# Kernel tuning notes

Hardware: AMD Instinct MI355X
Metric: run time of the kernel (lower is better)

Reference implementation:

```python
import jax, jax.numpy as jnp
import numpy as np

B, H, V, L = 4096, 1024, 64, 16  # batch, hidden_size, msg_vocsize, max_msg_len


def setup_inputs() -> dict:
    key = jax.random.key(0)
    ks = jax.random.split(key, 10)
    s = 1.0 / np.sqrt(H)
    return {
        "encoder_hidden": jax.random.normal(ks[0], (B, H), jnp.float32),
        "encoder_cell": jax.random.normal(ks[1], (B, H), jnp.float32),
        "W_ih": jax.random.uniform(ks[2], (4 * H, H), jnp.float32, -s, s),
        "W_hh": jax.random.uniform(ks[3], (4 * H, H), jnp.float32, -s, s),
        "b_ih": jax.random.uniform(ks[4], (4 * H,), jnp.float32, -s, s),
        "b_hh": jax.random.uniform(ks[5], (4 * H,), jnp.float32, -s, s),
        "W_out": jax.random.uniform(ks[6], (V, H), jnp.float32, -s, s),
        "b_out": jax.random.uniform(ks[7], (V,), jnp.float32, -s, s),
        "init_input": jnp.zeros((1, H), jnp.float32),  # nn.Parameter initialized to zeros
        "msg_embedding": jax.random.normal(ks[8], (V, H), jnp.float32),
    }


def reference(encoder_hidden, encoder_cell, W_ih, W_hh, b_ih, b_hh,
              W_out, b_out, init_input, msg_embedding):
    batch = encoder_hidden.shape[0]
    x0 = jnp.broadcast_to(init_input, (batch, H))

    def step(carry, _):
        h, c, x, logp = carry
        x = jax.nn.relu(x)
        gates = x @ W_ih.T + b_ih + h @ W_hh.T + b_hh  # [B, 4H]
        i, f, g, o = jnp.split(gates, 4, axis=-1)      # torch LSTMCell gate order
        i, f, o = jax.nn.sigmoid(i), jax.nn.sigmoid(f), jax.nn.sigmoid(o)
        g = jnp.tanh(g)
        c = f * c + i * g
        h = o * jnp.tanh(c)
        logits = h @ W_out.T + b_out                   # [B, V]
        probs = jax.nn.softmax(logits, axis=1)
        pred = jax.nn.one_hot(jnp.argmax(probs, axis=1), V, dtype=probs.dtype)
        logp = logp + jnp.log(jnp.sum(probs * pred, axis=1))
        x = pred @ msg_embedding                       # [B, H]
        return (h, c, x, logp), (pred, logits)

    init = (encoder_hidden, encoder_cell, x0, jnp.zeros((batch,), encoder_hidden.dtype))
    (_, _, _, log_probs), (message, digits) = jax.lax.scan(step, init, None, length=L)
    mask = jnp.ones((L, 1, batch), encoder_hidden.dtype)
    return message, mask, digits, log_probs
```

## Files before the change

### kernel.cpp

```cpp
#include <hip/hip_runtime.h>
#include <math.h>

#define HD    1024
#define BATCH 4096
#define VOC   64
#define MSGL  16
#define KH    1024
#define NG    4096

typedef _Float16 f16;
typedef _Float16 f16x8 __attribute__((ext_vector_type(8)));
typedef _Float16 f16x4 __attribute__((ext_vector_type(4)));
typedef float    f32x4 __attribute__((ext_vector_type(4)));

__device__ __forceinline__ void splt(float v, f16& hi, f16& lo) {
    f16 h = (f16)v;
    hi = h;
    lo = (f16)(v - (float)h);
}

__device__ __forceinline__ float sigm_f(float x) {
    return __builtin_amdgcn_rcpf(1.0f + __builtin_amdgcn_exp2f(-1.44269504088896f * x));
}
__device__ __forceinline__ float tanh_f(float x) {
    return 1.0f - 2.0f * __builtin_amdgcn_rcpf(1.0f + __builtin_amdgcn_exp2f(2.88539008177793f * x));
}

__device__ __forceinline__ int orig_n(int np) {
    const int bxx = np >> 8, rem = np & 255;
    const int jh = rem >> 6, g = (rem >> 4) & 3, cnn = rem & 15;
    return g * 1024 + bxx * 64 + jh * 16 + cnn;
}
__device__ __forceinline__ int j_of(int np) {
    const int bxx = np >> 8, rem = np & 255;
    const int jh = rem >> 6, cnn = rem & 15;
    return bxx * 64 + jh * 16 + cnn;
}

__device__ __forceinline__ void async16(void* lds, const void* g) {
    __builtin_amdgcn_global_load_lds(
        (const __attribute__((address_space(1))) void*)g,
        (__attribute__((address_space(3))) void*)lds, 16, 0, 0);
}

__device__ __forceinline__ int swz(int row, int gran) {
    return row * 128 + ((gran ^ (row & 7)) << 4);
}

__device__ __forceinline__ void stage(char* ldsbase, const f16* hi, const f16* lo,
                                      int gbase, int k0, int r, int tid) {
    const int o   = (r * 512 + tid) * 16;
    const int row = o >> 7;
    const int gp  = (o >> 4) & 7;
    const int g   = gp ^ (row & 7);
    const f16* src = (g < 4 ? hi : lo) + (size_t)(gbase + row) * KH + k0 + (g & 3) * 8;
    async16(ldsbase + o, src);
}

__global__ __launch_bounds__(512, 2) void gemm_fused(
    const f16* __restrict__ Hh, const f16* __restrict__ Hl,
    const f16* __restrict__ Whi, const f16* __restrict__ Wlo,
    const float* __restrict__ XG, const int* __restrict__ ambuf,
    float* __restrict__ cbuf,
    f16* __restrict__ HhN, f16* __restrict__ HlN, int t)
{
    __shared__ char smem[132096];
    __shared__ int sAm[256];

    const int tid  = threadIdx.x;
    const int lane = tid & 63;
    const int wv   = tid >> 6;
    const int wm   = wv >> 2;
    const int wn   = wv & 3;

    const int d  = blockIdx.x;
    const int xc = d & 7;
    const int i_ = d >> 3;
    const int by = xc + 8 * (i_ >> 4);
    const int bx = i_ & 15;
    const int bm   = by * 256;
    const int bnp  = bx * 256;
    const int rl   = lane & 15;
    const int kg   = lane >> 4;

    f32x4 acc[8][4];
#pragma unroll
    for (int i = 0; i < 8; ++i)
#pragma unroll
        for (int g = 0; g < 4; ++g) acc[i][g] = f32x4{0.f, 0.f, 0.f, 0.f};

    if (tid < 256) sAm[tid] = (t == 0) ? 64 : ambuf[bm + tid];

#pragma unroll
    for (int r = 0; r < 4; ++r) stage(smem,         Hh,  Hl,  bm,  0, r, tid);
#pragma unroll
    for (int r = 0; r < 4; ++r) stage(smem + 32768, Whi, Wlo, bnp, 0, r, tid);

    for (int kt = 0; kt < 32; ++kt) {
        const char* cb = smem + (kt & 1) * 65536;
        char* nb = smem + ((kt + 1) & 1) * 65536;
        const int kn = ((kt + 1) & 31) * 32;

        asm volatile("s_waitcnt vmcnt(4)" ::: "memory");
        asm volatile("s_barrier" ::: "memory");

#pragma unroll
        for (int r = 0; r < 4; ++r) stage(nb, Hh, Hl, bm, kn, r, tid);

        asm volatile("s_waitcnt vmcnt(4)" ::: "memory");
        asm volatile("s_barrier" ::: "memory");

        f16x8 bh[4], bl[4];
#pragma unroll
        for (int f = 0; f < 4; ++f) {
            const int row = wn * 64 + f * 16 + rl;
            bh[f] = *(const f16x8*)(cb + 32768 + swz(row, kg));
            bl[f] = *(const f16x8*)(cb + 32768 + swz(row, kg + 4));
        }
#pragma unroll
        for (int r = 0; r < 4; ++r) stage(nb + 32768, Whi, Wlo, bnp, kn, r, tid);

        __builtin_amdgcn_s_setprio(1);
#pragma unroll
        for (int f = 0; f < 8; ++f) {
            const int row = wm * 128 + f * 16 + rl;
            const f16x8 ah = *(const f16x8*)(cb + swz(row, kg));
            const f16x8 al = *(const f16x8*)(cb + swz(row, kg + 4));
#pragma unroll
            for (int g = 0; g < 4; ++g) {
                acc[f][g] = __builtin_amdgcn_mfma_f32_16x16x32_f16(ah, bh[g], acc[f][g], 0, 0, 0);
                acc[f][g] = __builtin_amdgcn_mfma_f32_16x16x32_f16(ah, bl[g], acc[f][g], 0, 0, 0);
                acc[f][g] = __builtin_amdgcn_mfma_f32_16x16x32_f16(al, bh[g], acc[f][g], 0, 0, 0);
            }
        }
        __builtin_amdgcn_s_setprio(0);
    }

    asm volatile("s_waitcnt vmcnt(0)" ::: "memory");
    __syncthreads();

    float* sXG = (float*)smem;
    f16*   hHi = (f16*)(smem + 66560);
    f16*   hLo = (f16*)(smem + 99328);
    const int jb = bx * 64;

#pragma unroll
    for (int i = 0; i < 9; ++i) {
        const int idx = i * 512 + tid;
        if (idx < 65 * 64) {
            const int v  = idx >> 6;
            const int c4 = (idx & 63) * 4;
            *(float4*)&sXG[v * 256 + c4] =
                *(const float4*)&XG[(size_t)v * NG + bnp + c4];
        }
    }
    __syncthreads();

    const int q    = lane >> 4;
    const int lcol = wn * 16 + rl;
    const int jglob = jb + lcol;
#pragma unroll
    for (int i = 0; i < 8; ++i) {
#pragma unroll
        for (int rg = 0; rg < 4; ++rg) {
            const int lrow = wm * 128 + i * 16 + q * 4 + rg;
            const int v = sAm[lrow];
            const float4 xg = *(const float4*)&sXG[v * 256 + lcol * 4];
            const size_t ci = (size_t)(bm + lrow) * HD + jglob;
            const float cold = cbuf[ci];
            const float I = sigm_f(acc[i][0][rg] + xg.x);
            const float F = sigm_f(acc[i][1][rg] + xg.y);
            const float G = tanh_f(acc[i][2][rg] + xg.z);
            const float O = sigm_f(acc[i][3][rg] + xg.w);
            const float cc = F * cold + I * G;
            const float hh = O * tanh_f(cc);
            cbuf[ci] = cc;
            f16 hi_, lo_;
            splt(hh, hi_, lo_);
            hHi[lrow * 64 + lcol] = hi_;
            hLo[lrow * 64 + lcol] = lo_;
        }
    }
    __syncthreads();

#pragma unroll
    for (int r = 0; r < 8; ++r) {
        const int idx = r * 512 + tid;
        const int row = idx >> 4;
        const int c4  = (idx & 15) * 4;
        *(f16x4*)&HhN[(size_t)(bm + row) * HD + jb + c4] = *(f16x4*)&hHi[row * 64 + c4];
        *(f16x4*)&HlN[(size_t)(bm + row) * HD + jb + c4] = *(f16x4*)&hLo[row * 64 + c4];
    }
}

__global__ __launch_bounds__(256) void logits_step(
    const f16* __restrict__ Hh, const f16* __restrict__ Hl,
    const float* __restrict__ W_outT, const float* __restrict__ b_out,
    float* __restrict__ omsg, float* __restrict__ odig,
    float* __restrict__ ologp, int* __restrict__ ambuf, int t)
{
    const int lane = threadIdx.x & 63;
    const int wv   = threadIdx.x >> 6;
    const int r0   = blockIdx.x * 8 + wv * 2;

    float a0 = 0.f, a1 = 0.f;
    const f16* hh0 = Hh + (size_t)r0 * HD;
    const f16* hl0 = Hl + (size_t)r0 * HD;
    const f16* hh1 = hh0 + HD;
    const f16* hl1 = hl0 + HD;
    for (int k = 0; k < HD; k += 4) {
        const float w0 = W_outT[(k + 0) * 64 + lane];
        const float w1 = W_outT[(k + 1) * 64 + lane];
        const float w2 = W_outT[(k + 2) * 64 + lane];
        const float w3 = W_outT[(k + 3) * 64 + lane];
        const f16x4 vh0 = *(const f16x4*)&hh0[k];
        const f16x4 vl0 = *(const f16x4*)&hl0[k];
        const f16x4 vh1 = *(const f16x4*)&hh1[k];
        const f16x4 vl1 = *(const f16x4*)&hl1[k];
        a0 += w0 * ((float)vh0[0] + (float)vl0[0]) + w1 * ((float)vh0[1] + (float)vl0[1])
            + w2 * ((float)vh0[2] + (float)vl0[2]) + w3 * ((float)vh0[3] + (float)vl0[3]);
        a1 += w0 * ((float)vh1[0] + (float)vl1[0]) + w1 * ((float)vh1[1] + (float)vl1[1])
            + w2 * ((float)vh1[2] + (float)vl1[2]) + w3 * ((float)vh1[3] + (float)vl1[3]);
    }
    const float bo = b_out[lane];
    const float accs[2] = {a0, a1};

#pragma unroll
    for (int r = 0; r < 2; ++r) {
        const int row = r0 + r;
        const float lg = accs[r] + bo;

        float m = lg; int am = lane;
#pragma unroll
        for (int d = 1; d < 64; d <<= 1) {
            const float om = __shfl_xor(m, d);
            const int   oa = __shfl_xor(am, d);
            if (om > m || (om == m && oa < am)) { m = om; am = oa; }
        }
        float s = expf(lg - m);
#pragma unroll
        for (int d = 1; d < 64; d <<= 1) s += __shfl_xor(s, d);

        odig[(size_t)row * VOC + lane] = lg;
        omsg[(size_t)row * VOC + lane] = (lane == am) ? 1.0f : 0.0f;
        if (lane == 0) {
            const float prev = (t == 0) ? 0.0f : ologp[row];
            ologp[row] = prev - logf(s);
            ambuf[row] = am;
        }
    }
}

__global__ __launch_bounds__(256) void xg_kernel(
    const float* __restrict__ W_ih, const float* __restrict__ rembT,
    const float* __restrict__ rembX0, const float* __restrict__ bR,
    float* __restrict__ XG)
{
    __shared__ float sW[4][1024];
    const int lane = threadIdx.x & 63;
    const int wv   = threadIdx.x >> 6;
    const int np   = blockIdx.x * 4 + wv;
    const int orig = orig_n(np);
    const float* wr = W_ih + (size_t)orig * HD;
#pragma unroll
    for (int c = 0; c < 4; ++c)
        *(float4*)&sW[wv][c * 256 + lane * 4] = *(const float4*)&wr[c * 256 + lane * 4];
    __syncthreads();

    float acc = 0.f, acc0 = 0.f;
#pragma unroll 4
    for (int k = 0; k < HD; ++k) {
        const float w = sW[wv][k];
        acc  += w * rembT[k * 64 + lane];
        acc0 += w * rembX0[k];
    }
    const float b = bR[np];
    const int g = (np >> 4) & 3;
    const int pos = j_of(np) * 4 + g;
    XG[(size_t)lane * NG + pos] = acc + b;
    if (lane == 0) XG[(size_t)64 * NG + pos] = acc0 + b;
}

__global__ __launch_bounds__(256) void prep_w(
    const float* __restrict__ W_hh, f16* __restrict__ Whi, f16* __restrict__ Wlo)
{
    const long long idx = ((long long)blockIdx.x * 256 + threadIdx.x) * 4;
    const int np = (int)(idx >> 10);
    const int k  = (int)(idx & 1023);
    const float4 v = *(const float4*)&W_hh[(size_t)orig_n(np) * HD + k];
    f16x4 vh, vl; f16 hi_, lo_;
    splt(v.x, hi_, lo_); vh[0] = hi_; vl[0] = lo_;
    splt(v.y, hi_, lo_); vh[1] = hi_; vl[1] = lo_;
    splt(v.z, hi_, lo_); vh[2] = hi_; vl[2] = lo_;
    splt(v.w, hi_, lo_); vh[3] = hi_; vl[3] = lo_;
    *(f16x4*)&Whi[idx] = vh;
    *(f16x4*)&Wlo[idx] = vl;
}

__global__ __launch_bounds__(256) void prep_h(
    const float* __restrict__ ench, f16* __restrict__ Hh, f16* __restrict__ Hl)
{
    const int idx = (blockIdx.x * 256 + threadIdx.x) * 4;
    const float4 v = *(const float4*)&ench[idx];
    f16x4 vh, vl; f16 hi_, lo_;
    splt(v.x, hi_, lo_); vh[0] = hi_; vl[0] = lo_;
    splt(v.y, hi_, lo_); vh[1] = hi_; vl[1] = lo_;
    splt(v.z, hi_, lo_); vh[2] = hi_; vl[2] = lo_;
    splt(v.w, hi_, lo_); vh[3] = hi_; vl[3] = lo_;
    *(f16x4*)&Hh[idx] = vh;
    *(f16x4*)&Hl[idx] = vl;
}

__global__ __launch_bounds__(256) void prep_c(
    const float* __restrict__ encc, float* __restrict__ cbuf)
{
    const int idx = (blockIdx.x * 256 + threadIdx.x) * 4;
    *(float4*)&cbuf[idx] = *(const float4*)&encc[idx];
}

__global__ __launch_bounds__(256) void prep_small(
    const float* __restrict__ W_out, const float* __restrict__ b_ih,
    const float* __restrict__ b_hh, const float* __restrict__ emb,
    const float* __restrict__ x0,
    float* __restrict__ W_outT, float* __restrict__ rembT,
    float* __restrict__ rembX0, float* __restrict__ bR, float* __restrict__ mask)
{
    const int i = blockIdx.x * 256 + threadIdx.x;
    mask[i] = 1.0f;
    const int v = i >> 10, k = i & 1023;
    W_outT[k * 64 + v] = W_out[i];
    rembT[k * 64 + v] = fmaxf(emb[i], 0.f);
    if (i < 1024) rembX0[i] = fmaxf(x0[i], 0.f);
    if (i < NG) {
        const int orig = orig_n(i);
        bR[i] = b_ih[orig] + b_hh[orig];
    }
}

extern "C" void kernel_launch(void* const* d_in, const int* in_sizes, int n_in,
                              void* d_out, int out_size, void* d_ws, size_t ws_size,
                              hipStream_t stream)
{
    const float* ench  = (const float*)d_in[0];
    const float* encc  = (const float*)d_in[1];
    const float* W_ih  = (const float*)d_in[2];
    const float* W_hh  = (const float*)d_in[3];
    const float* b_ih  = (const float*)d_in[4];
    const float* b_hh  = (const float*)d_in[5];
    const float* W_out = (const float*)d_in[6];
    const float* b_out = (const float*)d_in[7];
    const float* x0    = (const float*)d_in[8];
    const float* emb   = (const float*)d_in[9];
    float* out = (float*)d_out;

    char* ws = (char*)d_ws;
    f16*   Hh[2]  = { (f16*)(ws + ((size_t) 0 << 20)), (f16*)(ws + ((size_t)16 << 20)) };
    f16*   Hl[2]  = { (f16*)(ws + ((size_t) 8 << 20)), (f16*)(ws + ((size_t)24 << 20)) };
    f16*   Whr    = (f16*)(ws + ((size_t)32 << 20));
    f16*   Wlr    = (f16*)(ws + ((size_t)40 << 20));
    float* cbuf   = (float*)(ws + ((size_t)48 << 20));
    float* W_outT = (float*)(ws + ((size_t)64 << 20));
    float* rembT  = (float*)(ws + ((size_t)65 << 20));
    float* rembX0 = (float*)(ws + ((size_t)66 << 20));
    float* bR     = (float*)(ws + ((size_t)66 << 20) + 8192);
    float* XG     = (float*)(ws + ((size_t)67 << 20));
    int*   ambuf  = (int*)  (ws + ((size_t)69 << 20));

    float* out_msg0 = out;
    float* out_mask = out + (size_t)MSGL * BATCH * VOC;
    float* out_dig0 = out_mask + (size_t)MSGL * BATCH;
    float* out_logp = out_dig0 + (size_t)MSGL * BATCH * VOC;

    prep_w<<<4096, 256, 0, stream>>>(W_hh, Whr, Wlr);
    prep_h<<<4096, 256, 0, stream>>>(ench, Hh[0], Hl[0]);
    prep_c<<<4096, 256, 0, stream>>>(encc, cbuf);
    prep_small<<<256, 256, 0, stream>>>(W_out, b_ih, b_hh, emb, x0,
                                        W_outT, rembT, rembX0, bR, out_mask);
    xg_kernel<<<1024, 256, 0, stream>>>(W_ih, rembT, rembX0, bR, XG);

    for (int t = 0; t < MSGL; ++t) {
        const int cur = t & 1, nxt = cur ^ 1;
        gemm_fused<<<256, 512, 0, stream>>>(
            Hh[cur], Hl[cur], Whr, Wlr, XG, ambuf, cbuf, Hh[nxt], Hl[nxt], t);
        logits_step<<<512, 256, 0, stream>>>(
            Hh[nxt], Hl[nxt], W_outT, b_out,
            out_msg0 + (size_t)t * BATCH * VOC,
            out_dig0 + (size_t)t * BATCH * VOC,
            out_logp, ambuf, t);
    }
}
```

Baseline: 2.393 ms.

## Fuse all timesteps into one persistent cooperative kernel with grid syncs

Replaces the 32 per-step launches (GEMM+LSTM kernel and logits kernel) with a single cooperative kernel that loops over the 16 timesteps and uses grid.sync between the recurrent GEMM phase and the logits/argmax phase. This is meant to remove kernel launch gaps and tail effects. It also drops the XCD-aware block remapping and lowers launch bounds to one block per CU. The logits phase now runs on 256 blocks instead of 512, and grid-wide barriers add their own cost.

```diff
diff --git a/kernel.cpp b/kernel.cpp
--- a/kernel.cpp
+++ b/kernel.cpp
@@ -1,5 +1,8 @@
 #include <hip/hip_runtime.h>
+#include <hip/hip_cooperative_groups.h>
 #include <math.h>
+
+namespace cg = cooperative_groups;
 
 #define HD    1024
 #define BATCH 4096
@@ -57,13 +60,17 @@
     async16(ldsbase + o, src);
 }
 
-__global__ __launch_bounds__(512, 2) void gemm_fused(
-    const f16* __restrict__ Hh, const f16* __restrict__ Hl,
+__global__ __launch_bounds__(512, 1) void fused_loop(
+    f16* __restrict__ Hh0, f16* __restrict__ Hl0,
+    f16* __restrict__ Hh1, f16* __restrict__ Hl1,
     const f16* __restrict__ Whi, const f16* __restrict__ Wlo,
-    const float* __restrict__ XG, const int* __restrict__ ambuf,
+    const float* __restrict__ XG, int* __restrict__ ambuf,
     float* __restrict__ cbuf,
-    f16* __restrict__ HhN, f16* __restrict__ HlN, int t)
-{
+    const float* __restrict__ W_outT, const float* __restrict__ b_out,
+    float* __restrict__ omsg0, float* __restrict__ odig0,
+    float* __restrict__ ologp)
+{
+    cg::grid_group grid = cg::this_grid();
     __shared__ char smem[132096];
     __shared__ int sAm[256];
 
@@ -72,182 +79,188 @@
     const int wv   = tid >> 6;
     const int wm   = wv >> 2;
     const int wn   = wv & 3;
-
-    const int d  = blockIdx.x;
-    const int xc = d & 7;
-    const int i_ = d >> 3;
-    const int by = xc + 8 * (i_ >> 4);
-    const int bx = i_ & 15;
+    const int d    = blockIdx.x;
+    const int by   = d >> 4;
+    const int bx   = d & 15;
     const int bm   = by * 256;
     const int bnp  = bx * 256;
     const int rl   = lane & 15;
     const int kg   = lane >> 4;
 
-    f32x4 acc[8][4];
-#pragma unroll
-    for (int i = 0; i < 8; ++i)
-#pragma unroll
-        for (int g = 0; g < 4; ++g) acc[i][g] = f32x4{0.f, 0.f, 0.f, 0.f};
-
-    if (tid < 256) sAm[tid] = (t == 0) ? 64 : ambuf[bm + tid];
-
-#pragma unroll
-    for (int r = 0; r < 4; ++r) stage(smem,         Hh,  Hl,  bm,  0, r, tid);
-#pragma unroll
-    for (int r = 0; r < 4; ++r) stage(smem + 32768, Whi, Wlo, bnp, 0, r, tid);
-
-    for (int kt = 0; kt < 32; ++kt) {
-        const char* cb = smem + (kt & 1) * 65536;
-        char* nb = smem + ((kt + 1) & 1) * 65536;
-        const int kn = ((kt + 1) & 31) * 32;
-
-        asm volatile("s_waitcnt vmcnt(4)" ::: "memory");
-        asm volatile("s_barrier" ::: "memory");
-
-#pragma unroll
-        for (int r = 0; r < 4; ++r) stage(nb, Hh, Hl, bm, kn, r, tid);
-
-        asm volatile("s_waitcnt vmcnt(4)" ::: "memory");
-        asm volatile("s_barrier" ::: "memory");
-
-        f16x8 bh[4], bl[4];
-#pragma unroll
-        for (int f = 0; f < 4; ++f) {
-            const int row = wn * 64 + f * 16 + rl;
-            bh[f] = *(const f16x8*)(cb + 32768 + swz(row, kg));
-            bl[f] = *(const f16x8*)(cb + 32768 + swz(row, kg + 4));
+#pragma unroll 1
+    for (int t = 0; t < MSGL; ++t) {
+        const f16* Hh = (t & 1) ? Hh1 : Hh0;
+        const f16* Hl = (t & 1) ? Hl1 : Hl0;
+        f16* HhN = (t & 1) ? Hh0 : Hh1;
+        f16* HlN = (t & 1) ? Hl0 : Hl1;
+
+        f32x4 acc[8][4];
+#pragma unroll
+        for (int i = 0; i < 8; ++i)
+#pragma unroll
+            for (int g = 0; g < 4; ++g) acc[i][g] = f32x4{0.f, 0.f, 0.f, 0.f};
+
+        if (tid < 256) sAm[tid] = (t == 0) ? 64 : ambuf[bm + tid];
+
+#pragma unroll
+        for (int r = 0; r < 4; ++r) stage(smem,         Hh,  Hl,  bm,  0, r, tid);
+#pragma unroll
+        for (int r = 0; r < 4; ++r) stage(smem + 32768, Whi, Wlo, bnp, 0, r, tid);
+
+        for (int kt = 0; kt < 32; ++kt) {
+            const char* cb = smem + (kt & 1) * 65536;
+            char* nb = smem + ((kt + 1) & 1) * 65536;
+            const int kn = ((kt + 1) & 31) * 32;
+
+            asm volatile("s_waitcnt vmcnt(4)" ::: "memory");
+            asm volatile("s_barrier" ::: "memory");
+
+#pragma unroll
+            for (int r = 0; r < 4; ++r) stage(nb, Hh, Hl, bm, kn, r, tid);
+
+            asm volatile("s_waitcnt vmcnt(4)" ::: "memory");
+            asm volatile("s_barrier" ::: "memory");
+
+            f16x8 bh[4], bl[4];
+#pragma unroll
+            for (int f = 0; f < 4; ++f) {
+                const int row = wn * 64 + f * 16 + rl;
+                bh[f] = *(const f16x8*)(cb + 32768 + swz(row, kg));
+                bl[f] = *(const f16x8*)(cb + 32768 + swz(row, kg + 4));
+            }
+#pragma unroll
+            for (int r = 0; r < 4; ++r) stage(nb + 32768, Whi, Wlo, bnp, kn, r, tid);
+
+            __builtin_amdgcn_s_setprio(1);
+#pragma unroll
+            for (int f = 0; f < 8; ++f) {
+                const int row = wm * 128 + f * 16 + rl;
+                const f16x8 ah = *(const f16x8*)(cb + swz(row, kg));
+                const f16x8 al = *(const f16x8*)(cb + swz(row, kg + 4));
+#pragma unroll
+                for (int g = 0; g < 4; ++g) {
+                    acc[f][g] = __builtin_amdgcn_mfma_f32_16x16x32_f16(ah, bh[g], acc[f][g], 0, 0, 0);
+                    acc[f][g] = __builtin_amdgcn_mfma_f32_16x16x32_f16(ah, bl[g], acc[f][g], 0, 0, 0);
+                    acc[f][g] = __builtin_amdgcn_mfma_f32_16x16x32_f16(al, bh[g], acc[f][g], 0, 0, 0);
+                }
+            }
+            __builtin_amdgcn_s_setprio(0);
         }
-#pragma unroll
-        for (int r = 0; r < 4; ++r) stage(nb + 32768, Whi, Wlo, bnp, kn, r, tid);
-
-        __builtin_amdgcn_s_setprio(1);
-#pragma unroll
-        for (int f = 0; f < 8; ++f) {
-            const int row = wm * 128 + f * 16 + rl;
-            const f16x8 ah = *(const f16x8*)(cb + swz(row, kg));
-            const f16x8 al = *(const f16x8*)(cb + swz(row, kg + 4));
-#pragma unroll
-            for (int g = 0; g < 4; ++g) {
-                acc[f][g] = __builtin_amdgcn_mfma_f32_16x16x32_f16(ah, bh[g], acc[f][g], 0, 0, 0);
-                acc[f][g] = __builtin_amdgcn_mfma_f32_16x16x32_f16(ah, bl[g], acc[f][g], 0, 0, 0);
-                acc[f][g] = __builtin_amdgcn_mfma_f32_16x16x32_f16(al, bh[g], acc[f][g], 0, 0, 0);
+
+        asm volatile("s_waitcnt vmcnt(0)" ::: "memory");
+        __syncthreads();
+
+        float* sXG = (float*)smem;
+        f16*   hHi = (f16*)(smem + 66560);
+        f16*   hLo = (f16*)(smem + 99328);
+        const int jb = bx * 64;
+
+#pragma unroll
+        for (int i = 0; i < 9; ++i) {
+            const int idx = i * 512 + tid;
+            if (idx < 65 * 64) {
+                const int v  = idx >> 6;
+                const int c4 = (idx & 63) * 4;
+                *(float4*)&sXG[v * 256 + c4] =
+                    *(const float4*)&XG[(size_t)v * NG + bnp + c4];
             }
         }
-        __builtin_amdgcn_s_setprio(0);
-    }
-
-    asm volatile("s_waitcnt vmcnt(0)" ::: "memory");
-    __syncthreads();
-
-    float* sXG = (float*)smem;
-    f16*   hHi = (f16*)(smem + 66560);
-    f16*   hLo = (f16*)(smem + 99328);
-    const int jb = bx * 64;
-
-#pragma unroll
-    for (int i = 0; i < 9; ++i) {
-        const int idx = i * 512 + tid;
-        if (idx < 65 * 64) {
-            const int v  = idx >> 6;
-            const int c4 = (idx & 63) * 4;
-            *(float4*)&sXG[v * 256 + c4] =
-                *(const float4*)&XG[(size_t)v * NG + bnp + c4];
+        __syncthreads();
+
+        const int q    = lane >> 4;
+        const int lcol = wn * 16 + rl;
+        const int jglob = jb + lcol;
+#pragma unroll
+        for (int i = 0; i < 8; ++i) {
+#pragma unroll
+            for (int rg = 0; rg < 4; ++rg) {
+                const int lrow = wm * 128 + i * 16 + q * 4 + rg;
+                const int v = sAm[lrow];
+                const float4 xg = *(const float4*)&sXG[v * 256 + lcol * 4];
+                const size_t ci = (size_t)(bm + lrow) * HD + jglob;
+                const float cold = cbuf[ci];
+                const float I = sigm_f(acc[i][0][rg] + xg.x);
+                const float F = sigm_f(acc[i][1][rg] + xg.y);
+                const float G = tanh_f(acc[i][2][rg] + xg.z);
+                const float O = sigm_f(acc[i][3][rg] + xg.w);
+                const float cc = F * cold + I * G;
+                const float hh = O * tanh_f(cc);
+                cbuf[ci] = cc;
+                f16 hi_, lo_;
+                splt(hh, hi_, lo_);
+                hHi[lrow * 64 + lcol] = hi_;
+                hLo[lrow * 64 + lcol] = lo_;
+            }
         }
-    }
-    __syncthreads();
-
-    const int q    = lane >> 4;
-    const int lcol = wn * 16 + rl;
-    const int jglob = jb + lcol;
-#pragma unroll
-    for (int i = 0; i < 8; ++i) {
-#pragma unroll
-        for (int rg = 0; rg < 4; ++rg) {
-            const int lrow = wm * 128 + i * 16 + q * 4 + rg;
-            const int v = sAm[lrow];
-            const float4 xg = *(const float4*)&sXG[v * 256 + lcol * 4];
-            const size_t ci = (size_t)(bm + lrow) * HD + jglob;
-            const float cold = cbuf[ci];
-            const float I = sigm_f(acc[i][0][rg] + xg.x);
-            const float F = sigm_f(acc[i][1][rg] + xg.y);
-            const float G = tanh_f(acc[i][2][rg] + xg.z);
-            const float O = sigm_f(acc[i][3][rg] + xg.w);
-            const float cc = F * cold + I * G;
-            const float hh = O * tanh_f(cc);
-            cbuf[ci] = cc;
-            f16 hi_, lo_;
-            splt(hh, hi_, lo_);
-            hHi[lrow * 64 + lcol] = hi_;
-            hLo[lrow * 64 + lcol] = lo_;
+        __syncthreads();
+
+#pragma unroll
+        for (int r = 0; r < 8; ++r) {
+            const int idx = r * 512 + tid;
+            const int row = idx >> 4;
+            const int c4  = (idx & 15) * 4;
+            *(f16x4*)&HhN[(size_t)(bm + row) * HD + jb + c4] = *(f16x4*)&hHi[row * 64 + c4];
+            *(f16x4*)&HlN[(size_t)(bm + row) * HD + jb + c4] = *(f16x4*)&hLo[row * 64 + c4];
         }
-    }
-    __syncthreads();
-
-#pragma unroll
-    for (int r = 0; r < 8; ++r) {
-        const int idx = r * 512 + tid;
-        const int row = idx >> 4;
-        const int c4  = (idx & 15) * 4;
-        *(f16x4*)&HhN[(size_t)(bm + row) * HD + jb + c4] = *(f16x4*)&hHi[row * 64 + c4];
-        *(f16x4*)&HlN[(size_t)(bm + row) * HD + jb + c4] = *(f16x4*)&hLo[row * 64 + c4];
-    }
-}
-
-__global__ __launch_bounds__(256) void logits_step(
-    const f16* __restrict__ Hh, const f16* __restrict__ Hl,
-    const float* __restrict__ W_outT, const float* __restrict__ b_out,
-    float* __restrict__ omsg, float* __restrict__ odig,
-    float* __restrict__ ologp, int* __restrict__ ambuf, int t)
-{
-    const int lane = threadIdx.x & 63;
-    const int wv   = threadIdx.x >> 6;
-    const int r0   = blockIdx.x * 8 + wv * 2;
-
-    float a0 = 0.f, a1 = 0.f;
-    const f16* hh0 = Hh + (size_t)r0 * HD;
-    const f16* hl0 = Hl + (size_t)r0 * HD;
-    const f16* hh1 = hh0 + HD;
-    const f16* hl1 = hl0 + HD;
-    for (int k = 0; k < HD; k += 4) {
-        const float w0 = W_outT[(k + 0) * 64 + lane];
-        const float w1 = W_outT[(k + 1) * 64 + lane];
-        const float w2 = W_outT[(k + 2) * 64 + lane];
-        const float w3 = W_outT[(k + 3) * 64 + lane];
-        const f16x4 vh0 = *(const f16x4*)&hh0[k];
-        const f16x4 vl0 = *(const f16x4*)&hl0[k];
-        const f16x4 vh1 = *(const f16x4*)&hh1[k];
-        const f16x4 vl1 = *(const f16x4*)&hl1[k];
-        a0 += w0 * ((float)vh0[0] + (float)vl0[0]) + w1 * ((float)vh0[1] + (float)vl0[1])
-            + w2 * ((float)vh0[2] + (float)vl0[2]) + w3 * ((float)vh0[3] + (float)vl0[3]);
-        a1 += w0 * ((float)vh1[0] + (float)vl1[0]) + w1 * ((float)vh1[1] + (float)vl1[1])
-            + w2 * ((float)vh1[2] + (float)vl1[2]) + w3 * ((float)vh1[3] + (float)vl1[3]);
-    }
-    const float bo = b_out[lane];
-    const float accs[2] = {a0, a1};
-
-#pragma unroll
-    for (int r = 0; r < 2; ++r) {
-        const int row = r0 + r;
-        const float lg = accs[r] + bo;
-
-        float m = lg; int am = lane;
-#pragma unroll
-        for (int d = 1; d < 64; d <<= 1) {
-            const float om = __shfl_xor(m, d);
-            const int   oa = __shfl_xor(am, d);
-            if (om > m || (om == m && oa < am)) { m = om; am = oa; }
+
+        __threadfence();
+        grid.sync();
+
+        {
+            float* omsg = omsg0 + (size_t)t * BATCH * VOC;
+            float* odig = odig0 + (size_t)t * BATCH * VOC;
+            const int r0 = d * 16 + wv * 2;
+
+            float a0 = 0.f, a1 = 0.f;
+            const f16* hh0 = HhN + (size_t)r0 * HD;
+            const f16* hl0 = HlN + (size_t)r0 * HD;
+            const f16* hh1 = hh0 + HD;
+            const f16* hl1 = hl0 + HD;
+            for (int k = 0; k < HD; k += 4) {
+                const float w0 = W_outT[(k + 0) * 64 + lane];
+                const float w1 = W_outT[(k + 1) * 64 + lane];
+                const float w2 = W_outT[(k + 2) * 64 + lane];
+                const float w3 = W_outT[(k + 3) * 64 + lane];
+                const f16x4 vh0 = *(const f16x4*)&hh0[k];
+                const f16x4 vl0 = *(const f16x4*)&hl0[k];
+                const f16x4 vh1 = *(const f16x4*)&hh1[k];
+                const f16x4 vl1 = *(const f16x4*)&hl1[k];
+                a0 += w0 * ((float)vh0[0] + (float)vl0[0]) + w1 * ((float)vh0[1] + (float)vl0[1])
+                    + w2 * ((float)vh0[2] + (float)vl0[2]) + w3 * ((float)vh0[3] + (float)vl0[3]);
+                a1 += w0 * ((float)vh1[0] + (float)vl1[0]) + w1 * ((float)vh1[1] + (float)vl1[1])
+                    + w2 * ((float)vh1[2] + (float)vl1[2]) + w3 * ((float)vh1[3] + (float)vl1[3]);
+            }
+            const float bo = b_out[lane];
+            const float accs[2] = {a0, a1};
+
+#pragma unroll
+            for (int r = 0; r < 2; ++r) {
+                const int row = r0 + r;
+                const float lg = accs[r] + bo;
+
+                float m = lg; int am = lane;
+#pragma unroll
+                for (int dd = 1; dd < 64; dd <<= 1) {
+                    const float om = __shfl_xor(m, dd);
+                    const int   oa = __shfl_xor(am, dd);
+                    if (om > m || (om == m && oa < am)) { m = om; am = oa; }
+                }
+                float s = expf(lg - m);
+#pragma unroll
+                for (int dd = 1; dd < 64; dd <<= 1) s += __shfl_xor(s, dd);
+
+                odig[(size_t)row * VOC + lane] = lg;
+                omsg[(size_t)row * VOC + lane] = (lane == am) ? 1.0f : 0.0f;
+                if (lane == 0) {
+                    const float prev = (t == 0) ? 0.0f : ologp[row];
+                    ologp[row] = prev - logf(s);
+                    ambuf[row] = am;
+                }
+            }
         }
-        float s = expf(lg - m);
-#pragma unroll
-        for (int d = 1; d < 64; d <<= 1) s += __shfl_xor(s, d);
-
-        odig[(size_t)row * VOC + lane] = lg;
-        omsg[(size_t)row * VOC + lane] = (lane == am) ? 1.0f : 0.0f;
-        if (lane == 0) {
-            const float prev = (t == 0) ? 0.0f : ologp[row];
-            ologp[row] = prev - logf(s);
-            ambuf[row] = am;
-        }
+
+        __threadfence();
+        grid.sync();
     }
 }
 
@@ -354,8 +367,10 @@
     float* out = (float*)d_out;
 
     char* ws = (char*)d_ws;
-    f16*   Hh[2]  = { (f16*)(ws + ((size_t) 0 << 20)), (f16*)(ws + ((size_t)16 << 20)) };
-    f16*   Hl[2]  = { (f16*)(ws + ((size_t) 8 << 20)), (f16*)(ws + ((size_t)24 << 20)) };
+    f16*   Hh0    = (f16*)(ws + ((size_t) 0 << 20));
+    f16*   Hl0    = (f16*)(ws + ((size_t) 8 << 20));
+    f16*   Hh1    = (f16*)(ws + ((size_t)16 << 20));
+    f16*   Hl1    = (f16*)(ws + ((size_t)24 << 20));
     f16*   Whr    = (f16*)(ws + ((size_t)32 << 20));
     f16*   Wlr    = (f16*)(ws + ((size_t)40 << 20));
     float* cbuf   = (float*)(ws + ((size_t)48 << 20));
@@ -372,20 +387,18 @@
     float* out_logp = out_dig0 + (size_t)MSGL * BATCH * VOC;
 
     prep_w<<<4096, 256, 0, stream>>>(W_hh, Whr, Wlr);
-    prep_h<<<4096, 256, 0, stream>>>(ench, Hh[0], Hl[0]);
+    prep_h<<<4096, 256, 0, stream>>>(ench, Hh0, Hl0);
     prep_c<<<4096, 256, 0, stream>>>(encc, cbuf);
     prep_small<<<256, 256, 0, stream>>>(W_out, b_ih, b_hh, emb, x0,
                                         W_outT, rembT, rembX0, bR, out_mask);
     xg_kernel<<<1024, 256, 0, stream>>>(W_ih, rembT, rembX0, bR, XG);
 
-    for (int t = 0; t < MSGL; ++t) {
-        const int cur = t & 1, nxt = cur ^ 1;
-        gemm_fused<<<256, 512, 0, stream>>>(
-            Hh[cur], Hl[cur], Whr, Wlr, XG, ambuf, cbuf, Hh[nxt], Hl[nxt], t);
-        logits_step<<<512, 256, 0, stream>>>(
-            Hh[nxt], Hl[nxt], W_outT, b_out,
-            out_msg0 + (size_t)t * BATCH * VOC,
-            out_dig0 + (size_t)t * BATCH * VOC,
-            out_logp, ambuf, t);
-    }
-}
+    void* kargs[] = {
+        (void*)&Hh0, (void*)&Hl0, (void*)&Hh1, (void*)&Hl1,
+        (void*)&Whr, (void*)&Wlr, (void*)&XG, (void*)&ambuf,
+        (void*)&cbuf, (void*)&W_outT, (void*)&b_out,
+        (void*)&out_msg0, (void*)&out_dig0, (void*)&out_logp
+    };
+    hipLaunchCooperativeKernel((void*)fused_loop, dim3(256), dim3(512),
+                               kargs, 0, stream);
+}
```

New measurement: 5.717 ms. 2.39x slower.
